# Optimization experiments

Hardware: AMD Instinct MI355X
Metric: run time of the kernel (lower is better)

Reference implementation:

```python
import jax, jax.numpy as jnp
import numpy as np

N = 8192
D = 1024

def setup_inputs() -> dict:
    key = jax.random.key(0)
    ks = jax.random.split(key, 15)
    s = 1.0 / np.sqrt(D)
    def lin(kw, kb):
        W = jax.random.uniform(kw, (D, D), jnp.float32, -s, s)
        b = jax.random.uniform(kb, (D,), jnp.float32, -s, s)
        return W, b
    Wq, bq = lin(ks[0], ks[1])
    Wk, bk = lin(ks[2], ks[3])
    Wv, bv = lin(ks[4], ks[5])
    W1, b1 = lin(ks[6], ks[7])
    W2, b2 = lin(ks[8], ks[9])
    W3, b3 = lin(ks[10], ks[11])
    final_weight = jax.random.normal(ks[12], (D, 1), jnp.float32)
    x = jax.random.normal(ks[13], (N, D), jnp.float32)
    return {"x": x, "Wq": Wq, "bq": bq, "Wk": Wk, "bk": bk, "Wv": Wv, "bv": bv,
            "W1": W1, "b1": b1, "W2": W2, "b2": b2, "W3": W3, "b3": b3,
            "final_weight": final_weight}

def reference(x, Wq, bq, Wk, bk, Wv, bv, W1, b1, W2, b2, W3, b3, final_weight):
    # torch Linear: y = x @ W.T + b
    Q = x @ Wq.T + bq              # [N, D]
    K = x @ Wk.T + bk
    V = x @ Wv.T + bv
    scale = 1.0 / np.sqrt(x.shape[1]).astype(np.float32)
    scores = (Q @ K.T) * scale     # [N, N]
    attn = jax.nn.softmax(scores, axis=1)
    attended = attn @ V            # [N, D]
    out = jax.nn.relu(attended @ W1.T + b1)
    out = jax.nn.relu(out @ W2.T + b2)
    out = jax.nn.relu(out @ W3.T + b3)
    out = out @ final_weight       # [N, 1]
    return out.squeeze(-1)         # [N]
```

## Files before the change

### kernel.cpp

```cpp
#include <hip/hip_runtime.h>
#include <hip/hip_bf16.h>

typedef __bf16 bf16x8 __attribute__((ext_vector_type(8)));
typedef float f32x4 __attribute__((ext_vector_type(4)));
typedef int i32x4 __attribute__((ext_vector_type(4)));
typedef unsigned short us8 __attribute__((ext_vector_type(8)));
typedef unsigned short us4 __attribute__((ext_vector_type(4)));

__device__ inline float bf2f(unsigned short u) {
  union { unsigned u; float f; } x; x.u = ((unsigned)u) << 16; return x.f;
}
__device__ inline unsigned short f2bf(float f) {
  union { float f; unsigned u; } x; x.f = f;
  unsigned r = x.u + 0x7fffu + ((x.u >> 16) & 1u);
  return (unsigned short)(r >> 16);
}

__device__ inline unsigned xcd_chunk(unsigned b, unsigned nwg) {
  const unsigned x = b & 7u, idx = b >> 3;
  const unsigned q = nwg >> 3, r = nwg & 7u;
  const unsigned base = (x < r) ? x * (q + 1u) : r * (q + 1u) + (x - r) * q;
  return base + idx;
}

__global__ __launch_bounds__(256) void cast_f32_bf16(
    const float* __restrict__ src, unsigned short* __restrict__ dst, int n4) {
  int i = blockIdx.x * 256 + threadIdx.x;
  if (i >= n4) return;
  float4 f = ((const float4*)src)[i];
  us4 u;
  u[0] = f2bf(f.x); u[1] = f2bf(f.y); u[2] = f2bf(f.z); u[3] = f2bf(f.w);
  *(us4*)&dst[i * 4] = u;
}

#define GLLDS(g, l) __builtin_amdgcn_global_load_lds( \
    (const __attribute__((address_space(1))) void*)(g), \
    (__attribute__((address_space(3))) void*)(l), 16, 0, 0)
#define LGKM0  asm volatile("s_waitcnt lgkmcnt(0)" ::: "memory")

__global__ __launch_bounds__(256)
void gemm_s_i8(const signed char* __restrict__ A,
               const signed char* __restrict__ B,
               float scale, signed char* __restrict__ C,
               float* __restrict__ part,
               int M, int N, int K, int ldc) {
  __shared__ __align__(16) signed char lds[2][2][8192];
  const int tid = threadIdx.x;
  const int wave = tid >> 6, lane = tid & 63;
  const int wm = wave >> 1, wn = wave & 1;
  const unsigned gx = gridDim.x, nwg = gx * gridDim.y;
  const unsigned w = xcd_chunk(blockIdx.y * gx + blockIdx.x, nwg);
  const long m0 = (long)(w / gx) * 128, n0 = (long)(w % gx) * 128;

  i32x4 acc[4][4];
#pragma unroll
  for (int i = 0; i < 4; ++i)
#pragma unroll
    for (int j = 0; j < 4; ++j) acc[i][j] = (i32x4){0, 0, 0, 0};

  const int srow = tid >> 2;
  const int scol = (tid & 3) * 16;
#pragma unroll
  for (int j = 0; j < 2; ++j) {
    GLLDS(A + (m0 + j * 64 + srow) * (long)K + scol, &lds[0][0][j * 4096 + wave * 1024]);
    GLLDS(B + (n0 + j * 64 + srow) * (long)K + scol, &lds[0][1][j * 4096 + wave * 1024]);
  }

  const int lr = lane & 15;
  const int lk16 = (lane >> 4) * 16;
  const int KT = K >> 6;
  int cur = 0;
  for (int kt = 0; kt < KT; ++kt) {
    __syncthreads();
    if (kt + 1 < KT) {
      const long k0 = (long)(kt + 1) << 6;
#pragma unroll
      for (int j = 0; j < 2; ++j) {
        GLLDS(A + (m0 + j * 64 + srow) * (long)K + k0 + scol, &lds[cur ^ 1][0][j * 4096 + wave * 1024]);
        GLLDS(B + (n0 + j * 64 + srow) * (long)K + k0 + scol, &lds[cur ^ 1][1][j * 4096 + wave * 1024]);
      }
    }
    i32x4 af[4], bfr[4];
#pragma unroll
    for (int i = 0; i < 4; ++i)
      af[i] = *(const i32x4*)&lds[cur][0][(wm * 64 + i * 16 + lr) * 64 + lk16];
#pragma unroll
    for (int j = 0; j < 4; ++j)
      bfr[j] = *(const i32x4*)&lds[cur][1][(wn * 64 + j * 16 + lr) * 64 + lk16];
#pragma unroll
    for (int i = 0; i < 4; ++i)
#pragma unroll
      for (int j = 0; j < 4; ++j)
        acc[i][j] = __builtin_amdgcn_mfma_i32_16x16x64_i8(af[i], bfr[j], acc[i][j], 0, 0, 0);
    cur ^= 1;
  }

  __syncthreads();
  unsigned short* eps = (unsigned short*)&lds[0][0][0] + (size_t)wave * 4096;
  const int cc = lane & 15, cr = (lane >> 4) * 4;
#pragma unroll
  for (int i = 0; i < 4; ++i) {
    float s4[4] = {0.f, 0.f, 0.f, 0.f};
#pragma unroll
    for (int j = 0; j < 4; ++j) {
      const int colp = j * 16 + cc;
      const i32x4 v = acc[i][j];
#pragma unroll
      for (int r = 0; r < 4; ++r) {
        const int row = i * 16 + cr + r;
        const float e = __expf((float)v[r] * scale);
        const float qf = (float)__float2int_rn(fminf(e * 15.875f, 127.0f));
        s4[r] += qf;
        const int phys = ((colp >> 3) ^ (row & 7)) * 8 + (colp & 7);
        eps[row * 64 + phys] = f2bf(qf);
      }
    }
#pragma unroll
    for (int r = 0; r < 4; ++r)
#pragma unroll
      for (int o = 1; o < 16; o <<= 1) s4[r] += __shfl_xor(s4[r], o);
    if ((lane & 15) == 0) {
      const long row = m0 + wm * 64 + i * 16 + cr;
      const long pidx = (n0 >> 7) * 2 + wn;
#pragma unroll
      for (int r = 0; r < 4; ++r) part[pidx * (long)M + row + r] = s4[r];
    }
  }
  LGKM0;
#pragma unroll
  for (int p = 0; p < 4; ++p) {
    const int prow = p * 16 + (lane >> 2);
    const int slot = lane & 3;
#pragma unroll
    for (int gi = 0; gi < 2; ++gi) {
      const int grp = gi * 4 + slot;
      us8 vv = *(const us8*)&eps[prow * 64 + ((grp ^ (prow & 7)) * 8)];
      unsigned lo = 0, hi = 0;
#pragma unroll
      for (int j = 0; j < 4; ++j) lo |= ((unsigned)(int)bf2f(vv[j]) & 0xffu) << (8 * j);
#pragma unroll
      for (int j = 0; j < 4; ++j) hi |= ((unsigned)(int)bf2f(vv[4 + j]) & 0xffu) << (8 * j);
      const long grow = m0 + wm * 64 + prow;
      const long gcol = n0 + wn * 64 + grp * 8;
      uint2 pk; pk.x = lo; pk.y = hi;
      *(uint2*)&C[grow * (long)ldc + gcol] = pk;
    }
  }
}

__global__ __launch_bounds__(256) void reduce_rowinv(const float* __restrict__ part,
                                                     float* __restrict__ inv, int M, float dq) {
  const int row = blockIdx.x * 256 + threadIdx.x;
  float s = 0.f;
#pragma unroll 8
  for (int p = 0; p < 128; ++p) s += part[(long)p * M + row];
  inv[row] = dq / s;
}

__global__ __launch_bounds__(256)
void gemm_pv_i8(const signed char* __restrict__ A,
                const signed char* __restrict__ B,
                const float* __restrict__ rowscale,
                unsigned short* __restrict__ C,
                int M, int N, int K, int ldc) {
  __shared__ __align__(16) signed char lds[2][2][8192];
  const int tid = threadIdx.x;
  const int wave = tid >> 6, lane = tid & 63;
  const int wm = wave >> 1, wn = wave & 1;
  const unsigned gx = gridDim.x, nwg = gx * gridDim.y;
  const unsigned w = xcd_chunk(blockIdx.y * gx + blockIdx.x, nwg);
  const long m0 = (long)(w / gx) * 128, n0 = (long)(w % gx) * 128;

  i32x4 acc[4][4];
#pragma unroll
  for (int i = 0; i < 4; ++i)
#pragma unroll
    for (int j = 0; j < 4; ++j) acc[i][j] = (i32x4){0, 0, 0, 0};

  const int srow = tid >> 2;
  const int scol = (tid & 3) * 16;
#pragma unroll
  for (int j = 0; j < 2; ++j) {
    GLLDS(A + (m0 + j * 64 + srow) * (long)K + scol, &lds[0][0][j * 4096 + wave * 1024]);
    GLLDS(B + (n0 + j * 64 + srow) * (long)K + scol, &lds[0][1][j * 4096 + wave * 1024]);
  }

  const int lr = lane & 15;
  const int lk16 = (lane >> 4) * 16;
  const int KT = K >> 6;
  int cur = 0;
  for (int kt = 0; kt < KT; ++kt) {
    __syncthreads();
    if (kt + 1 < KT) {
      const long k0 = (long)(kt + 1) << 6;
#pragma unroll
      for (int j = 0; j < 2; ++j) {
        GLLDS(A + (m0 + j * 64 + srow) * (long)K + k0 + scol, &lds[cur ^ 1][0][j * 4096 + wave * 1024]);
        GLLDS(B + (n0 + j * 64 + srow) * (long)K + k0 + scol, &lds[cur ^ 1][1][j * 4096 + wave * 1024]);
      }
    }
    i32x4 af[4], bfr[4];
#pragma unroll
    for (int i = 0; i < 4; ++i)
      af[i] = *(const i32x4*)&lds[cur][0][(wm * 64 + i * 16 + lr) * 64 + lk16];
#pragma unroll
    for (int j = 0; j < 4; ++j)
      bfr[j] = *(const i32x4*)&lds[cur][1][(wn * 64 + j * 16 + lr) * 64 + lk16];
#pragma unroll
    for (int i = 0; i < 4; ++i)
#pragma unroll
      for (int j = 0; j < 4; ++j)
        acc[i][j] = __builtin_amdgcn_mfma_i32_16x16x64_i8(af[i], bfr[j], acc[i][j], 0, 0, 0);
    cur ^= 1;
  }

  const int cc = lane & 15, cr = (lane >> 4) * 4;
#pragma unroll
  for (int i = 0; i < 4; ++i) {
#pragma unroll
    for (int j = 0; j < 4; ++j) {
      const long grow = m0 + wm * 64 + i * 16 + cr;
      const long gcol = n0 + wn * 64 + j * 16 + cc;
      const i32x4 v = acc[i][j];
#pragma unroll
      for (int r = 0; r < 4; ++r)
        C[(grow + r) * (long)ldc + gcol] = f2bf((float)v[r] * rowscale[grow + r]);
    }
  }
}

template<int EPI>
__global__ __launch_bounds__(256)
void gemm_bt(const unsigned short* __restrict__ A,
             const unsigned short* __restrict__ B,
             const float* __restrict__ bias, float p1,
             unsigned short* __restrict__ C,
             int M, int N, int K, int ldc) {
  __shared__ unsigned short lds[2][2][4096];
  const int tid = threadIdx.x;
  const int wave = tid >> 6, lane = tid & 63;
  const int wm = wave >> 1, wn = wave & 1;
  const unsigned gx = gridDim.x, nwg = gx * gridDim.y;
  const unsigned w = xcd_chunk(blockIdx.y * gx + blockIdx.x, nwg);
  const long m0 = (long)(w / gx) * 128, n0 = (long)(w % gx) * 128;

  f32x4 acc[4][4];
#pragma unroll
  for (int i = 0; i < 4; ++i)
#pragma unroll
    for (int j = 0; j < 4; ++j) acc[i][j] = (f32x4){0.f, 0.f, 0.f, 0.f};

  const int srow = tid >> 2;
  const int scol = (tid & 3) * 8;
#pragma unroll
  for (int j = 0; j < 2; ++j) {
    const unsigned short* ga = A + (m0 + j * 64 + srow) * K + scol;
    const unsigned short* gb = B + (n0 + j * 64 + srow) * K + scol;
    GLLDS(ga, &lds[0][0][j * 2048 + wave * 512]);
    GLLDS(gb, &lds[0][1][j * 2048 + wave * 512]);
  }

  const int lr = lane & 15;
  const int lk = (lane >> 4) * 8;
  const int KT = K >> 5;
  int cur = 0;
  for (int kt = 0; kt < KT; ++kt) {
    __syncthreads();
    if (kt + 1 < KT) {
      const int k0 = (kt + 1) << 5;
#pragma unroll
      for (int j = 0; j < 2; ++j) {
        const unsigned short* ga = A + (m0 + j * 64 + srow) * K + k0 + scol;
        const unsigned short* gb = B + (n0 + j * 64 + srow) * K + k0 + scol;
        GLLDS(ga, &lds[cur ^ 1][0][j * 2048 + wave * 512]);
        GLLDS(gb, &lds[cur ^ 1][1][j * 2048 + wave * 512]);
      }
    }
    bf16x8 af[4], bfr[4];
#pragma unroll
    for (int i = 0; i < 4; ++i)
      af[i] = *(const bf16x8*)&lds[cur][0][(wm * 64 + i * 16 + lr) * 32 + lk];
#pragma unroll
    for (int j = 0; j < 4; ++j)
      bfr[j] = *(const bf16x8*)&lds[cur][1][(wn * 64 + j * 16 + lr) * 32 + lk];
#pragma unroll
    for (int i = 0; i < 4; ++i)
#pragma unroll
      for (int j = 0; j < 4; ++j)
        acc[i][j] = __builtin_amdgcn_mfma_f32_16x16x32_bf16(af[i], bfr[j], acc[i][j], 0, 0, 0);
    cur ^= 1;
  }

  const int cc = lane & 15, cr = (lane >> 4) * 4;
#pragma unroll
  for (int i = 0; i < 4; ++i) {
#pragma unroll
    for (int j = 0; j < 4; ++j) {
      const long grow = m0 + wm * 64 + i * 16 + cr;
      const long gcol = n0 + wn * 64 + j * 16 + cc;
      f32x4 v = acc[i][j];
      if constexpr (EPI == 2) {
        const float b = bias[gcol];
#pragma unroll
        for (int r = 0; r < 4; ++r)
          C[(grow + r) * (long)ldc + gcol] = f2bf(fmaxf(v[r] + b, 0.f));
      } else if constexpr (EPI == 5) {
        const float b = bias[gcol];
        signed char* Ci = (signed char*)C;
#pragma unroll
        for (int r = 0; r < 4; ++r) {
          int q = __float2int_rn((v[r] + b) * p1);
          q = q > 127 ? 127 : (q < -127 ? -127 : q);
          Ci[(grow + r) * (long)ldc + gcol] = (signed char)q;
        }
      } else {
        const float b = bias[gcol];
        signed char* Ci = (signed char*)C;
        unsigned pk = 0;
#pragma unroll
        for (int r = 0; r < 4; ++r) {
          int q = __float2int_rn((v[r] + b) * p1);
          q = q > 127 ? 127 : (q < -127 ? -127 : q);
          pk |= ((unsigned)q & 0xffu) << (8 * r);
        }
        *(unsigned*)&Ci[gcol * (long)ldc + grow] = pk;
      }
    }
  }
}

__global__ __launch_bounds__(256) void final_dot(const unsigned short* __restrict__ H,
                                                 const float* __restrict__ w,
                                                 float* __restrict__ out) {
  const int lane = threadIdx.x & 63, wave = threadIdx.x >> 6;
  const int row = blockIdx.x * 4 + wave;
  const unsigned short* h = H + (size_t)row * 1024;
  float s = 0.f;
#pragma unroll
  for (int k = 0; k < 2; ++k) {
    const int base = (lane + k * 64) * 8;
    us8 u = *(const us8*)&h[base];
#pragma unroll
    for (int r = 0; r < 8; ++r) s += bf2f(u[r]) * w[base + r];
  }
#pragma unroll
  for (int o = 32; o; o >>= 1) s += __shfl_xor(s, o);
  if (lane == 0) out[row] = s;
}

extern "C" void kernel_launch(void* const* d_in, const int* in_sizes, int n_in,
                              void* d_out, int out_size, void* d_ws, size_t ws_size,
                              hipStream_t stream) {
  const float* x  = (const float*)d_in[0];
  const float* Wq = (const float*)d_in[1];
  const float* bq = (const float*)d_in[2];
  const float* Wk = (const float*)d_in[3];
  const float* bk = (const float*)d_in[4];
  const float* Wv = (const float*)d_in[5];
  const float* bv = (const float*)d_in[6];
  const float* W1 = (const float*)d_in[7];
  const float* b1 = (const float*)d_in[8];
  const float* W2 = (const float*)d_in[9];
  const float* b2 = (const float*)d_in[10];
  const float* W3 = (const float*)d_in[11];
  const float* b3 = (const float*)d_in[12];
  const float* fw = (const float*)d_in[13];
  float* out = (float*)d_out;

  const int N = 8192, D = 1024;
  char* ws = (char*)d_ws;
  signed char* Si8 = (signed char*)ws;
  unsigned short* xb  = (unsigned short*)(ws + (size_t)N * N * 2);
  unsigned short* Qb  = xb + (size_t)N * D;
  unsigned short* Kb  = Qb + (size_t)N * D;
  unsigned short* Vt  = Kb + (size_t)N * D;
  unsigned short* Wqb = Vt + (size_t)N * D;
  unsigned short* Wkb = Wqb + (size_t)D * D;
  unsigned short* Wvb = Wkb + (size_t)D * D;
  unsigned short* W1b = Wvb + (size_t)D * D;
  unsigned short* W2b = W1b + (size_t)D * D;
  unsigned short* W3b = W2b + (size_t)D * D;
  float* part   = (float*)(W3b + (size_t)D * D);
  float* rowinv = part + (size_t)128 * N;
  signed char* Qi8 = (signed char*)Qb;
  signed char* Ki8 = (signed char*)Kb;
  signed char* Vti8 = (signed char*)Vt;
  unsigned short* att = xb;
  unsigned short* H1  = Qb;
  unsigned short* H2  = Kb;
  unsigned short* H3  = Vt;

  cast_f32_bf16<<<(N * D / 4 + 255) / 256, 256, 0, stream>>>(x, xb, N * D / 4);
  cast_f32_bf16<<<(D * D / 4 + 255) / 256, 256, 0, stream>>>(Wq, Wqb, D * D / 4);
  cast_f32_bf16<<<(D * D / 4 + 255) / 256, 256, 0, stream>>>(Wk, Wkb, D * D / 4);
  cast_f32_bf16<<<(D * D / 4 + 255) / 256, 256, 0, stream>>>(Wv, Wvb, D * D / 4);
  cast_f32_bf16<<<(D * D / 4 + 255) / 256, 256, 0, stream>>>(W1, W1b, D * D / 4);
  cast_f32_bf16<<<(D * D / 4 + 255) / 256, 256, 0, stream>>>(W2, W2b, D * D / 4);
  cast_f32_bf16<<<(D * D / 4 + 255) / 256, 256, 0, stream>>>(W3, W3b, D * D / 4);

  const dim3 blk(256);
  gemm_bt<5><<<dim3(D / 128, N / 128), blk, 0, stream>>>(xb, Wqb, bq, 31.75f, Qb, N, D, D, D);
  gemm_bt<5><<<dim3(D / 128, N / 128), blk, 0, stream>>>(xb, Wkb, bk, 31.75f, Kb, N, D, D, D);
  gemm_bt<6><<<dim3(D / 128, N / 128), blk, 0, stream>>>(xb, Wvb, bv, 31.75f, Vt, N, D, D, N);
  const float dq = 4.0f / 127.0f;
  gemm_s_i8<<<dim3(N / 128, N / 128), blk, 0, stream>>>(
      Qi8, Ki8, dq * dq / 32.0f, Si8, part, N, N, D, N);
  reduce_rowinv<<<N / 256, 256, 0, stream>>>(part, rowinv, N, dq);
  gemm_pv_i8<<<dim3(D / 128, N / 128), blk, 0, stream>>>(Si8, Vti8, rowinv, att, N, D, N, D);
  gemm_bt<2><<<dim3(D / 128, N / 128), blk, 0, stream>>>(att, W1b, b1, 0.f, H1, N, D, D, D);
  gemm_bt<2><<<dim3(D / 128, N / 128), blk, 0, stream>>>(H1, W2b, b2, 0.f, H2, N, D, D, D);
  gemm_bt<2><<<dim3(D / 128, N / 128), blk, 0, stream>>>(H2, W3b, b3, 0.f, H3, N, D, D, D);
  final_dot<<<N / 4, 256, 0, stream>>>(H3, fw, out);
}
```

Baseline: 369.9 us.

## Rewrite QK^T int8 GEMM with 256x256 tiles, 16 waves and interleaved staging

```diff
diff --git a/kernel.cpp b/kernel.cpp
--- a/kernel.cpp
+++ b/kernel.cpp
@@ -36,21 +36,26 @@
 #define GLLDS(g, l) __builtin_amdgcn_global_load_lds( \
     (const __attribute__((address_space(1))) void*)(g), \
     (__attribute__((address_space(3))) void*)(l), 16, 0, 0)
+#define VMCNT2 asm volatile("s_waitcnt vmcnt(2)" ::: "memory")
 #define LGKM0  asm volatile("s_waitcnt lgkmcnt(0)" ::: "memory")
-
-__global__ __launch_bounds__(256)
-void gemm_s_i8(const signed char* __restrict__ A,
-               const signed char* __restrict__ B,
-               float scale, signed char* __restrict__ C,
-               float* __restrict__ part,
-               int M, int N, int K, int ldc) {
-  __shared__ __align__(16) signed char lds[2][2][8192];
-  const int tid = threadIdx.x;
-  const int wave = tid >> 6, lane = tid & 63;
-  const int wm = wave >> 1, wn = wave & 1;
+#define BAR    __builtin_amdgcn_s_barrier()
+#define SCHED0 __builtin_amdgcn_sched_barrier(0)
+
+__global__ __launch_bounds__(1024, 1)
+void gemm256exp_i8(const signed char* __restrict__ A,
+                   const signed char* __restrict__ B,
+                   float c1, float c2, signed char* __restrict__ C,
+                   float* __restrict__ part,
+                   int M, int N, int K, int ldc) {
+  __shared__ __align__(16) signed char lds[131072];
+  const int tid = threadIdx.x, wave = tid >> 6, lane = tid & 63;
+  const int wm = wave >> 2, wn = wave & 3;
   const unsigned gx = gridDim.x, nwg = gx * gridDim.y;
   const unsigned w = xcd_chunk(blockIdx.y * gx + blockIdx.x, nwg);
-  const long m0 = (long)(w / gx) * 128, n0 = (long)(w % gx) * 128;
+  const long m0 = (long)(w / gx) * 256, n0 = (long)(w % gx) * 256;
+
+  signed char* ldsA0 = lds;
+  signed char* ldsB0 = lds + 65536;
 
   i32x4 acc[4][4];
 #pragma unroll
@@ -58,72 +63,115 @@
 #pragma unroll
     for (int j = 0; j < 4; ++j) acc[i][j] = (i32x4){0, 0, 0, 0};
 
-  const int srow = tid >> 2;
-  const int scol = (tid & 3) * 16;
-#pragma unroll
-  for (int j = 0; j < 2; ++j) {
-    GLLDS(A + (m0 + j * 64 + srow) * (long)K + scol, &lds[0][0][j * 4096 + wave * 1024]);
-    GLLDS(B + (n0 + j * 64 + srow) * (long)K + scol, &lds[0][1][j * 4096 + wave * 1024]);
-  }
-
-  const int lr = lane & 15;
-  const int lk16 = (lane >> 4) * 16;
-  const int KT = K >> 6;
-  int cur = 0;
+  const int srow = tid >> 3;
+  const int scol = ((tid & 7) ^ (srow & 7)) * 16;
+  const signed char* gA = A + (m0 + srow) * (long)K + scol;
+  const signed char* gB = B + (n0 + srow) * (long)K + scol;
+
+  auto stageA = [&](int buf, int h, long kb) {
+    GLLDS(gA + (long)(h * 128) * K + kb, ldsA0 + buf * 32768 + h * 16384 + wave * 1024);
+  };
+  auto stageB = [&](int buf, int h, long kb) {
+    GLLDS(gB + (long)(h * 128) * K + kb, ldsB0 + buf * 32768 + h * 16384 + wave * 1024);
+  };
+
+  const int lr = lane & 15, l7 = lane & 7, lk = lane >> 4;
+  i32x4 a[2][2], b0[2][2], b1[2][2];
+  auto readA = [&](int buf, int h) {
+#pragma unroll
+    for (int rf = 0; rf < 2; ++rf) {
+      const int row = wm * 32 + rf * 16 + lr;
+#pragma unroll
+      for (int ks = 0; ks < 2; ++ks)
+        a[rf][ks] = *(const i32x4*)&ldsA0[buf * 32768 + h * 16384 + row * 128 +
+                                          (((ks * 4 + lk) ^ l7) * 16)];
+    }
+  };
+  auto readB = [&](int buf, int h, i32x4 (&b)[2][2]) {
+#pragma unroll
+    for (int cf = 0; cf < 2; ++cf) {
+      const int row = wn * 32 + cf * 16 + lr;
+#pragma unroll
+      for (int ks = 0; ks < 2; ++ks)
+        b[cf][ks] = *(const i32x4*)&ldsB0[buf * 32768 + h * 16384 + row * 128 +
+                                          (((ks * 4 + lk) ^ l7) * 16)];
+    }
+  };
+  auto mfmaQ = [&](i32x4 (&av)[2][2], i32x4 (&bv)[2][2], int mh, int nh) {
+    __builtin_amdgcn_s_setprio(1);
+#pragma unroll
+    for (int rf = 0; rf < 2; ++rf)
+#pragma unroll
+      for (int cf = 0; cf < 2; ++cf)
+#pragma unroll
+        for (int ks = 0; ks < 2; ++ks)
+          acc[mh * 2 + rf][nh * 2 + cf] = __builtin_amdgcn_mfma_i32_16x16x64_i8(
+              av[rf][ks], bv[cf][ks], acc[mh * 2 + rf][nh * 2 + cf], 0, 0, 0);
+    __builtin_amdgcn_s_setprio(0);
+  };
+
+  stageA(0, 0, 0); stageB(0, 0, 0); stageB(0, 1, 0); stageA(0, 1, 0);
+
+  const int KT = K >> 7;
   for (int kt = 0; kt < KT; ++kt) {
-    __syncthreads();
-    if (kt + 1 < KT) {
-      const long k0 = (long)(kt + 1) << 6;
-#pragma unroll
-      for (int j = 0; j < 2; ++j) {
-        GLLDS(A + (m0 + j * 64 + srow) * (long)K + k0 + scol, &lds[cur ^ 1][0][j * 4096 + wave * 1024]);
-        GLLDS(B + (n0 + j * 64 + srow) * (long)K + k0 + scol, &lds[cur ^ 1][1][j * 4096 + wave * 1024]);
+    const int cur = kt & 1, nxt = cur ^ 1;
+    const long kn = (long)(kt + 1) << 7;
+    const bool more = (kt + 1 < KT);
+    VMCNT2; BAR; SCHED0;
+    readA(cur, 0); readB(cur, 0, b0);
+    if (more) stageA(nxt, 0, kn);
+    BAR; LGKM0; SCHED0;
+    mfmaQ(a, b0, 0, 0);
+    VMCNT2; BAR; SCHED0;
+    readB(cur, 1, b1);
+    if (more) stageB(nxt, 0, kn);
+    BAR; LGKM0; SCHED0;
+    mfmaQ(a, b1, 0, 1);
+    VMCNT2; BAR; SCHED0;
+    readA(cur, 1);
+    if (more) stageB(nxt, 1, kn);
+    BAR; LGKM0; SCHED0;
+    mfmaQ(a, b1, 1, 1);
+    BAR; SCHED0;
+    if (more) stageA(nxt, 1, kn);
+    BAR; SCHED0;
+    mfmaQ(a, b0, 1, 0);
+  }
+
+  BAR;
+  unsigned short* eps = (unsigned short*)lds + (size_t)wave * 4096;
+  const int cc = lane & 15, cr = (lane >> 4) * 4;
+#pragma unroll
+  for (int i = 0; i < 4; ++i) {
+    const int rbase = (i >> 1) * 32 + (i & 1) * 16 + cr;
+    float s2[2][4] = {{0.f, 0.f, 0.f, 0.f}, {0.f, 0.f, 0.f, 0.f}};
+#pragma unroll
+    for (int j = 0; j < 4; ++j) {
+      const int colp = (j >> 1) * 32 + (j & 1) * 16 + cc;
+      const i32x4 v = acc[i][j];
+#pragma unroll
+      for (int r = 0; r < 4; ++r) {
+        const int row = rbase + r;
+        const int q = __float2int_rn(fminf(exp2f(fmaf((float)v[r], c1, c2)), 127.0f));
+        s2[j >> 1][r] += (float)q;
+        const int phys = ((colp >> 3) ^ (row & 7)) * 8 + (colp & 7);
+        eps[row * 64 + phys] = (unsigned short)q;
       }
     }
-    i32x4 af[4], bfr[4];
-#pragma unroll
-    for (int i = 0; i < 4; ++i)
-      af[i] = *(const i32x4*)&lds[cur][0][(wm * 64 + i * 16 + lr) * 64 + lk16];
-#pragma unroll
-    for (int j = 0; j < 4; ++j)
-      bfr[j] = *(const i32x4*)&lds[cur][1][(wn * 64 + j * 16 + lr) * 64 + lk16];
-#pragma unroll
-    for (int i = 0; i < 4; ++i)
-#pragma unroll
-      for (int j = 0; j < 4; ++j)
-        acc[i][j] = __builtin_amdgcn_mfma_i32_16x16x64_i8(af[i], bfr[j], acc[i][j], 0, 0, 0);
-    cur ^= 1;
-  }
-
-  __syncthreads();
-  unsigned short* eps = (unsigned short*)&lds[0][0][0] + (size_t)wave * 4096;
-  const int cc = lane & 15, cr = (lane >> 4) * 4;
-#pragma unroll
-  for (int i = 0; i < 4; ++i) {
-    float s4[4] = {0.f, 0.f, 0.f, 0.f};
-#pragma unroll
-    for (int j = 0; j < 4; ++j) {
-      const int colp = j * 16 + cc;
-      const i32x4 v = acc[i][j];
-#pragma unroll
-      for (int r = 0; r < 4; ++r) {
-        const int row = i * 16 + cr + r;
-        const float e = __expf((float)v[r] * scale);
-        const float qf = (float)__float2int_rn(fminf(e * 15.875f, 127.0f));
-        s4[r] += qf;
-        const int phys = ((colp >> 3) ^ (row & 7)) * 8 + (colp & 7);
-        eps[row * 64 + phys] = f2bf(qf);
+#pragma unroll
+    for (int ch = 0; ch < 2; ++ch)
+#pragma unroll
+      for (int r = 0; r < 4; ++r)
+#pragma unroll
+        for (int o = 1; o < 16; o <<= 1) s2[ch][r] += __shfl_xor(s2[ch][r], o);
+    if ((lane & 15) == 0) {
+      const long grow = m0 + (long)(i >> 1) * 128 + wm * 32 + (i & 1) * 16 + cr;
+#pragma unroll
+      for (int ch = 0; ch < 2; ++ch) {
+        const long pidx = (n0 >> 8) * 8 + wn * 2 + ch;
+#pragma unroll
+        for (int r = 0; r < 4; ++r) part[pidx * (long)M + grow + r] = s2[ch][r];
       }
-    }
-#pragma unroll
-    for (int r = 0; r < 4; ++r)
-#pragma unroll
-      for (int o = 1; o < 16; o <<= 1) s4[r] += __shfl_xor(s4[r], o);
-    if ((lane & 15) == 0) {
-      const long row = m0 + wm * 64 + i * 16 + cr;
-      const long pidx = (n0 >> 7) * 2 + wn;
-#pragma unroll
-      for (int r = 0; r < 4; ++r) part[pidx * (long)M + row + r] = s4[r];
     }
   }
   LGKM0;
@@ -137,11 +185,11 @@
       us8 vv = *(const us8*)&eps[prow * 64 + ((grp ^ (prow & 7)) * 8)];
       unsigned lo = 0, hi = 0;
 #pragma unroll
-      for (int j = 0; j < 4; ++j) lo |= ((unsigned)(int)bf2f(vv[j]) & 0xffu) << (8 * j);
-#pragma unroll
-      for (int j = 0; j < 4; ++j) hi |= ((unsigned)(int)bf2f(vv[4 + j]) & 0xffu) << (8 * j);
-      const long grow = m0 + wm * 64 + prow;
-      const long gcol = n0 + wn * 64 + grp * 8;
+      for (int j = 0; j < 4; ++j) lo |= ((unsigned)vv[j] & 0xffu) << (8 * j);
+#pragma unroll
+      for (int j = 0; j < 4; ++j) hi |= ((unsigned)vv[4 + j] & 0xffu) << (8 * j);
+      const long grow = m0 + (long)(prow >> 5) * 128 + wm * 32 + (prow & 31);
+      const long gcol = n0 + (long)(grp >> 2) * 128 + wn * 32 + (grp & 3) * 8;
       uint2 pk; pk.x = lo; pk.y = hi;
       *(uint2*)&C[grow * (long)ldc + gcol] = pk;
     }
@@ -153,7 +201,7 @@
   const int row = blockIdx.x * 256 + threadIdx.x;
   float s = 0.f;
 #pragma unroll 8
-  for (int p = 0; p < 128; ++p) s += part[(long)p * M + row];
+  for (int p = 0; p < 256; ++p) s += part[(long)p * M + row];
   inv[row] = dq / s;
 }
 
@@ -381,7 +429,7 @@
   unsigned short* W2b = W1b + (size_t)D * D;
   unsigned short* W3b = W2b + (size_t)D * D;
   float* part   = (float*)(W3b + (size_t)D * D);
-  float* rowinv = part + (size_t)128 * N;
+  float* rowinv = part + (size_t)256 * N;
   signed char* Qi8 = (signed char*)Qb;
   signed char* Ki8 = (signed char*)Kb;
   signed char* Vti8 = (signed char*)Vt;
@@ -403,8 +451,10 @@
   gemm_bt<5><<<dim3(D / 128, N / 128), blk, 0, stream>>>(xb, Wkb, bk, 31.75f, Kb, N, D, D, D);
   gemm_bt<6><<<dim3(D / 128, N / 128), blk, 0, stream>>>(xb, Wvb, bv, 31.75f, Vt, N, D, D, N);
   const float dq = 4.0f / 127.0f;
-  gemm_s_i8<<<dim3(N / 128, N / 128), blk, 0, stream>>>(
-      Qi8, Ki8, dq * dq / 32.0f, Si8, part, N, N, D, N);
+  const float c1 = (dq * dq / 32.0f) * 1.4426950408889634f;
+  const float c2 = 3.9886846f;
+  gemm256exp_i8<<<dim3(N / 256, N / 256), dim3(1024), 0, stream>>>(
+      Qi8, Ki8, c1, c2, Si8, part, N, N, D, N);
   reduce_rowinv<<<N / 256, 256, 0, stream>>>(part, rowinv, N, dq);
   gemm_pv_i8<<<dim3(D / 128, N / 128), blk, 0, stream>>>(Si8, Vti8, rowinv, att, N, D, N, D);
   gemm_bt<2><<<dim3(D / 128, N / 128), blk, 0, stream>>>(att, W1b, b1, 0.f, H1, N, D, D, D);
```

After: 437.0 us. 18.1% more time.

## Widen QK^T int8 GEMM to 128x256 tiles with 512 threads and swizzled LDS

Applied to the files above, without the earlier changes.

```diff
diff --git a/kernel.cpp b/kernel.cpp
--- a/kernel.cpp
+++ b/kernel.cpp
@@ -36,21 +36,23 @@
 #define GLLDS(g, l) __builtin_amdgcn_global_load_lds( \
     (const __attribute__((address_space(1))) void*)(g), \
     (__attribute__((address_space(3))) void*)(l), 16, 0, 0)
+#define VMCNT3 asm volatile("s_waitcnt vmcnt(3)" ::: "memory")
+#define VMCNT0 asm volatile("s_waitcnt vmcnt(0)" ::: "memory")
 #define LGKM0  asm volatile("s_waitcnt lgkmcnt(0)" ::: "memory")
-
-__global__ __launch_bounds__(256)
+#define BAR    __builtin_amdgcn_s_barrier()
+
+__global__ __launch_bounds__(512, 4)
 void gemm_s_i8(const signed char* __restrict__ A,
                const signed char* __restrict__ B,
-               float scale, signed char* __restrict__ C,
+               float c1, float c2, signed char* __restrict__ C,
                float* __restrict__ part,
                int M, int N, int K, int ldc) {
-  __shared__ __align__(16) signed char lds[2][2][8192];
-  const int tid = threadIdx.x;
-  const int wave = tid >> 6, lane = tid & 63;
-  const int wm = wave >> 1, wn = wave & 1;
+  __shared__ __align__(16) signed char lds[65536];
+  const int tid = threadIdx.x, wave = tid >> 6, lane = tid & 63;
+  const int wm = wave >> 2, wn = wave & 3;
   const unsigned gx = gridDim.x, nwg = gx * gridDim.y;
   const unsigned w = xcd_chunk(blockIdx.y * gx + blockIdx.x, nwg);
-  const long m0 = (long)(w / gx) * 128, n0 = (long)(w % gx) * 128;
+  const long m0 = (long)(w / gx) * 128, n0 = (long)(w % gx) * 256;
 
   i32x4 acc[4][4];
 #pragma unroll
@@ -59,44 +61,44 @@
     for (int j = 0; j < 4; ++j) acc[i][j] = (i32x4){0, 0, 0, 0};
 
   const int srow = tid >> 2;
-  const int scol = (tid & 3) * 16;
-#pragma unroll
-  for (int j = 0; j < 2; ++j) {
-    GLLDS(A + (m0 + j * 64 + srow) * (long)K + scol, &lds[0][0][j * 4096 + wave * 1024]);
-    GLLDS(B + (n0 + j * 64 + srow) * (long)K + scol, &lds[0][1][j * 4096 + wave * 1024]);
-  }
-
-  const int lr = lane & 15;
-  const int lk16 = (lane >> 4) * 16;
+  const int scol = ((tid & 3) ^ ((srow >> 1) & 3)) * 16;
+  const signed char* gA = A + (m0 + srow) * (long)K + scol;
+  const signed char* gB = B + (n0 + srow) * (long)K + scol;
+
+  auto stage = [&](int buf, long kb) {
+    GLLDS(gA + kb, lds + buf * 8192 + tid * 16);
+    GLLDS(gB + kb, lds + 16384 + buf * 16384 + tid * 16);
+    GLLDS(gB + (long)128 * K + kb, lds + 16384 + buf * 16384 + 8192 + tid * 16);
+  };
+
+  const int lr = lane & 15, lk = lane >> 4;
   const int KT = K >> 6;
-  int cur = 0;
+  stage(0, 0);
   for (int kt = 0; kt < KT; ++kt) {
-    __syncthreads();
-    if (kt + 1 < KT) {
-      const long k0 = (long)(kt + 1) << 6;
-#pragma unroll
-      for (int j = 0; j < 2; ++j) {
-        GLLDS(A + (m0 + j * 64 + srow) * (long)K + k0 + scol, &lds[cur ^ 1][0][j * 4096 + wave * 1024]);
-        GLLDS(B + (n0 + j * 64 + srow) * (long)K + k0 + scol, &lds[cur ^ 1][1][j * 4096 + wave * 1024]);
-      }
-    }
-    i32x4 af[4], bfr[4];
+    const int cur = kt & 1;
+    if (kt + 1 < KT) { stage(cur ^ 1, (long)(kt + 1) << 6); VMCNT3; }
+    else             { VMCNT0; }
+    BAR;
+    i32x4 a[4], b[4];
+#pragma unroll
+    for (int f = 0; f < 4; ++f) {
+      const int row = wm * 64 + f * 16 + lr;
+      a[f] = *(const i32x4*)&lds[cur * 8192 + row * 64 + ((lk ^ ((row >> 1) & 3)) * 16)];
+    }
+#pragma unroll
+    for (int g = 0; g < 4; ++g) {
+      const int row = wn * 64 + g * 16 + lr;
+      b[g] = *(const i32x4*)&lds[16384 + cur * 16384 + row * 64 + ((lk ^ ((row >> 1) & 3)) * 16)];
+    }
 #pragma unroll
     for (int i = 0; i < 4; ++i)
-      af[i] = *(const i32x4*)&lds[cur][0][(wm * 64 + i * 16 + lr) * 64 + lk16];
-#pragma unroll
-    for (int j = 0; j < 4; ++j)
-      bfr[j] = *(const i32x4*)&lds[cur][1][(wn * 64 + j * 16 + lr) * 64 + lk16];
-#pragma unroll
-    for (int i = 0; i < 4; ++i)
 #pragma unroll
       for (int j = 0; j < 4; ++j)
-        acc[i][j] = __builtin_amdgcn_mfma_i32_16x16x64_i8(af[i], bfr[j], acc[i][j], 0, 0, 0);
-    cur ^= 1;
-  }
-
-  __syncthreads();
-  unsigned short* eps = (unsigned short*)&lds[0][0][0] + (size_t)wave * 4096;
+        acc[i][j] = __builtin_amdgcn_mfma_i32_16x16x64_i8(a[i], b[j], acc[i][j], 0, 0, 0);
+    BAR;
+  }
+
+  unsigned short* eps = (unsigned short*)lds + (size_t)wave * 4096;
   const int cc = lane & 15, cr = (lane >> 4) * 4;
 #pragma unroll
   for (int i = 0; i < 4; ++i) {
@@ -108,11 +110,10 @@
 #pragma unroll
       for (int r = 0; r < 4; ++r) {
         const int row = i * 16 + cr + r;
-        const float e = __expf((float)v[r] * scale);
-        const float qf = (float)__float2int_rn(fminf(e * 15.875f, 127.0f));
-        s4[r] += qf;
+        const int q = __float2int_rn(fminf(exp2f(fmaf((float)v[r], c1, c2)), 127.0f));
+        s4[r] += (float)q;
         const int phys = ((colp >> 3) ^ (row & 7)) * 8 + (colp & 7);
-        eps[row * 64 + phys] = f2bf(qf);
+        eps[row * 64 + phys] = (unsigned short)q;
       }
     }
 #pragma unroll
@@ -121,7 +122,7 @@
       for (int o = 1; o < 16; o <<= 1) s4[r] += __shfl_xor(s4[r], o);
     if ((lane & 15) == 0) {
       const long row = m0 + wm * 64 + i * 16 + cr;
-      const long pidx = (n0 >> 7) * 2 + wn;
+      const long pidx = (n0 >> 8) * 4 + wn;
 #pragma unroll
       for (int r = 0; r < 4; ++r) part[pidx * (long)M + row + r] = s4[r];
     }
@@ -137,9 +138,9 @@
       us8 vv = *(const us8*)&eps[prow * 64 + ((grp ^ (prow & 7)) * 8)];
       unsigned lo = 0, hi = 0;
 #pragma unroll
-      for (int j = 0; j < 4; ++j) lo |= ((unsigned)(int)bf2f(vv[j]) & 0xffu) << (8 * j);
-#pragma unroll
-      for (int j = 0; j < 4; ++j) hi |= ((unsigned)(int)bf2f(vv[4 + j]) & 0xffu) << (8 * j);
+      for (int j = 0; j < 4; ++j) lo |= ((unsigned)vv[j] & 0xffu) << (8 * j);
+#pragma unroll
+      for (int j = 0; j < 4; ++j) hi |= ((unsigned)vv[4 + j] & 0xffu) << (8 * j);
       const long grow = m0 + wm * 64 + prow;
       const long gcol = n0 + wn * 64 + grp * 8;
       uint2 pk; pk.x = lo; pk.y = hi;
@@ -403,8 +404,10 @@
   gemm_bt<5><<<dim3(D / 128, N / 128), blk, 0, stream>>>(xb, Wkb, bk, 31.75f, Kb, N, D, D, D);
   gemm_bt<6><<<dim3(D / 128, N / 128), blk, 0, stream>>>(xb, Wvb, bv, 31.75f, Vt, N, D, D, N);
   const float dq = 4.0f / 127.0f;
-  gemm_s_i8<<<dim3(N / 128, N / 128), blk, 0, stream>>>(
-      Qi8, Ki8, dq * dq / 32.0f, Si8, part, N, N, D, N);
+  const float c1 = (dq * dq / 32.0f) * 1.4426950408889634f;
+  const float c2 = 3.9886846f;
+  gemm_s_i8<<<dim3(N / 256, N / 128), dim3(512), 0, stream>>>(
+      Qi8, Ki8, c1, c2, Si8, part, N, N, D, N);
   reduce_rowinv<<<N / 256, 256, 0, stream>>>(part, rowinv, N, dq);
   gemm_pv_i8<<<dim3(D / 128, N / 128), blk, 0, stream>>>(Si8, Vti8, rowinv, att, N, D, N, D);
   gemm_bt<2><<<dim3(D / 128, N / 128), blk, 0, stream>>>(att, W1b, b1, 0.f, H1, N, D, D, D);
```

Result: faster. 359.1 us (-2.9%).
